# Kernel optimization log

Measured on AMD Instinct MI355X. Metric: run time of the kernel, lower is better.

Reference implementation:

```python
import jax, jax.numpy as jnp
import numpy as np

B, LP, LQ, D = 32, 2048, 512, 256

def setup_inputs() -> dict:
    key = jax.random.key(0)
    k1, k2, k3, k4 = jax.random.split(key, 4)
    x = jax.random.normal(k1, (B, LP, D), dtype=jnp.float32)
    y = jax.random.normal(k2, (B, LQ, D), dtype=jnp.float32)
    # nn.Linear(input_size, input_size): weight [D, D], bias [D]
    bound = 1.0 / np.sqrt(D)
    W = jax.random.uniform(k3, (D, D), minval=-bound, maxval=bound, dtype=jnp.float32)
    b = jax.random.uniform(k4, (D,), minval=-bound, maxval=bound, dtype=jnp.float32)
    return {"x": x, "y": y, "W": W, "b": b}

def reference(x, y, W, b):
    # shared linear + relu projection (torch Linear: x @ W.T + b)
    x_proj = jax.nn.relu(jnp.einsum('bpd,ed->bpe', x, W) + b)  # [B, LP, D]
    y_proj = jax.nn.relu(jnp.einsum('bqd,ed->bqe', y, W) + b)  # [B, LQ, D]
    # unscaled cross-attention scores
    scores = jnp.einsum('bpd,bqd->bpq', x_proj, y_proj)        # [B, LP, LQ]
    alpha = jax.nn.softmax(scores, axis=-1)
    # weighted sum over original (unprojected) y
    match_seq = jnp.einsum('bpq,bqd->bpd', alpha, y)           # [B, LP, D]
    return match_seq
```

## Files before the change

kernel.cpp:

```cpp
#include <hip/hip_runtime.h>
#include <stdint.h>

#define B_  32
#define LP_ 2048
#define LQ_ 512
#define D_  256

typedef __attribute__((ext_vector_type(8))) short short8;
typedef __attribute__((ext_vector_type(8))) _Float16 f16x8;
typedef __attribute__((ext_vector_type(4))) float f32x4;

__device__ __forceinline__ ushort f2h(float x) {
    union { _Float16 h; ushort u; } v;
    v.h = (_Float16)x;
    return v.u;
}
__device__ __forceinline__ void gl_lds16(const void* g, void* l) {
    __builtin_amdgcn_global_load_lds(
        (const __attribute__((address_space(1))) void*)g,
        (__attribute__((address_space(3))) void*)l, 16, 0, 0);
}


__global__ void k_prep(const float* __restrict__ W, const float* __restrict__ y,
                       ushort* __restrict__ Whf, ushort* __restrict__ yf) {
    __shared__ float t[32 * 260];
    if (blockIdx.x < 256) {
        int i = blockIdx.x * 256 + threadIdx.x;
        int e = i >> 8, k = i & 255;
        size_t off = (size_t)((k >> 5) * 16 + (e >> 4)) * 512 +
                     ((k >> 3) & 3) * 128 + (e & 15) * 8 + (k & 7);
        Whf[off] = f2h(W[i]);
        return;
    }
    int bid = blockIdx.x - 256;
    int b = bid >> 4, qc = bid & 15;
    int tid = threadIdx.x;
    int ql = tid >> 3;
    int d0 = (tid & 7) * 4;
#pragma unroll
    for (int p = 0; p < 8; p++) {
        int d = p * 32 + d0;
        float4 v = *(const float4*)(y + ((size_t)(b * LQ_ + qc * 32 + ql) * 256 + d));
        t[ql * 260 + d + 0] = v.x; t[ql * 260 + d + 1] = v.y;
        t[ql * 260 + d + 2] = v.z; t[ql * 260 + d + 3] = v.w;
    }
    __syncthreads();
    int w = tid >> 6, L = tid & 63, c = L & 15, quad = L >> 4;
#pragma unroll
    for (int ii = 0; ii < 4; ii++) {
        int nt = w * 4 + ii;
        short8 o;
#pragma unroll
        for (int j = 0; j < 8; j++)
            o[j] = (short)f2h(t[(quad * 8 + j) * 260 + nt * 16 + c]);
        *(short8*)(yf + ((size_t)(b * 256 + qc * 16 + nt) * 512 + L * 8)) = o;
    }
}

__global__ __launch_bounds__(256, 3) void k_proj(const float* __restrict__ x,
                                                 const float* __restrict__ y,
                                                 const ushort* __restrict__ Whf,
                                                 const float* __restrict__ bias,
                                                 ushort* __restrict__ Ox,
                                                 ushort* __restrict__ Oy) {
    __shared__ __align__(16) ushort Ws[16704];
    const int tid  = threadIdx.x;
    const int w    = tid >> 6;
    const int L    = tid & 63;
    const int c    = L & 15;
    const int quad = L >> 4;
    const bool isY = blockIdx.x < 256;
    const float* A = isY ? y : x;
    ushort* O      = isY ? Oy : Ox;
    const int blk0 = isY ? blockIdx.x : (blockIdx.x - 256);
    const int row0 = blk0 * 64 + w * 16;
    const int arow = row0 + c;

    f32x4 acc[16];
#pragma unroll
    for (int i = 0; i < 16; i++) acc[i] = (f32x4)0.f;

#define PSTAGE(kc, p)                                                          \
    {                                                                          \
        _Pragma("unroll")                                                      \
        for (int ii = 0; ii < 4; ii++) {                                       \
            int i = w * 4 + ii;                                                \
            gl_lds16(Whf + (size_t)(kc) * 8192 + i * 512 + L * 8,              \
                     (char*)Ws + (p) * 16384 + i * 1024);                      \
        }                                                                      \
    }

    PSTAGE(0, 0);
    float4 nx0 = *(const float4*)(A + (size_t)arow * 256 + quad * 8);
    float4 nx1 = *(const float4*)(A + (size_t)arow * 256 + quad * 8 + 4);

    for (int kc = 0; kc < 8; kc++) {
        __syncthreads();
        if (kc < 7) PSTAGE(kc + 1, (kc + 1) & 1);
        float4 cx0 = nx0, cx1 = nx1;
        if (kc < 7) {
            nx0 = *(const float4*)(A + (size_t)arow * 256 + (kc + 1) * 32 + quad * 8);
            nx1 = *(const float4*)(A + (size_t)arow * 256 + (kc + 1) * 32 + quad * 8 + 4);
        }
        float xs[8] = {cx0.x, cx0.y, cx0.z, cx0.w, cx1.x, cx1.y, cx1.z, cx1.w};
        f16x8 ah;
#pragma unroll
        for (int j = 0; j < 8; j++) ah[j] = (_Float16)xs[j];
        const ushort* buf = Ws + (kc & 1) * 8192;
#pragma unroll
        for (int nt = 0; nt < 16; nt++) {
            f16x8 bh = *(const f16x8*)(buf + nt * 512 + L * 8);
            acc[nt] = __builtin_amdgcn_mfma_f32_16x16x32_f16(ah, bh, acc[nt], 0, 0, 0);
        }
    }

    __syncthreads();
    float* tr = (float*)Ws + w * (16 * 130);
    const int rt_g = row0 >> 4;
#pragma unroll
    for (int half = 0; half < 2; half++) {
#pragma unroll
        for (int nt8 = 0; nt8 < 8; nt8++) {
            int nt = half * 8 + nt8;
            float bv = bias[nt * 16 + c];
#pragma unroll
            for (int r = 0; r < 4; r++)
                tr[(quad * 4 + r) * 130 + nt8 * 16 + c] = fmaxf(acc[nt][r] + bv, 0.f);
        }
#pragma unroll
        for (int ec4 = 0; ec4 < 4; ec4++) {
            int ec = half * 4 + ec4;
            short8 hh;
#pragma unroll
            for (int j = 0; j < 8; j++)
                hh[j] = (short)f2h(tr[c * 130 + ec4 * 32 + quad * 8 + j]);
            size_t blk = isY ? ((size_t)(rt_g >> 5) * 256 + ec * 32 + (rt_g & 31))
                             : ((size_t)rt_g * 8 + ec);
            *(short8*)(O + blk * 512 + L * 8) = hh;
        }
    }
}

__global__ __launch_bounds__(256, 4) void k_attn(const ushort* __restrict__ xpf,
                                                 const ushort* __restrict__ ypf,
                                                 const ushort* __restrict__ yf,
                                                 float* __restrict__ out) {
    __shared__ __align__(16) ushort lds[16384];
    const int tid  = threadIdx.x;
    const int w    = tid >> 6;
    const int L    = tid & 63;
    const int c    = L & 15;
    const int quad = L >> 4;

    const int bid = blockIdx.x;
    const int jj  = bid >> 3;
    const int b   = (bid & 7) * 4 + (jj >> 6);
    const int mt  = jj & 63;
    const int m0  = mt * 32;

#pragma unroll
    for (int ii = 0; ii < 4; ii++) {
        int unit = w * 4 + ii;
        int rs = unit >> 3, kc = unit & 7;
        gl_lds16(xpf + ((size_t)(b * 128 + mt * 2 + rs) * 8 + kc) * 512 + L * 8,
                 (char*)lds + unit * 1024);
    }

    f32x4 sc[2][8];
#pragma unroll
    for (int rs = 0; rs < 2; rs++)
#pragma unroll
        for (int qt = 0; qt < 8; qt++) sc[rs][qt] = (f32x4)0.f;
    __syncthreads();

    const ushort* yb = ypf + (size_t)b * 256 * 512;
    for (int kc = 0; kc < 8; kc++) {
        f16x8 ah0 = *(const f16x8*)(lds + kc * 512 + L * 8);
        f16x8 ah1 = *(const f16x8*)(lds + (8 + kc) * 512 + L * 8);
#pragma unroll
        for (int qt = 0; qt < 8; qt++) {
            f16x8 bh = *(const f16x8*)(yb + ((size_t)kc * 32 + w * 8 + qt) * 512 + L * 8);
            sc[0][qt] = __builtin_amdgcn_mfma_f32_16x16x32_f16(ah0, bh, sc[0][qt], 0, 0, 0);
            sc[1][qt] = __builtin_amdgcn_mfma_f32_16x16x32_f16(ah1, bh, sc[1][qt], 0, 0, 0);
        }
    }

    __syncthreads();
    float* red  = (float*)lds;
    float* red2 = red + 128;
    float inv[2][4];
#pragma unroll
    for (int rs = 0; rs < 2; rs++)
#pragma unroll
        for (int r = 0; r < 4; r++) {
            float pm = sc[rs][0][r];
#pragma unroll
            for (int qt = 1; qt < 8; qt++) pm = fmaxf(pm, sc[rs][qt][r]);
#pragma unroll
            for (int mask = 1; mask <= 8; mask <<= 1) pm = fmaxf(pm, __shfl_xor(pm, mask));
            if (c == 0) red[(rs * 16 + quad * 4 + r) * 4 + w] = pm;
        }
    __syncthreads();
#pragma unroll
    for (int rs = 0; rs < 2; rs++)
#pragma unroll
        for (int r = 0; r < 4; r++) {
            int row = rs * 16 + quad * 4 + r;
            float m = fmaxf(fmaxf(red[row * 4], red[row * 4 + 1]),
                            fmaxf(red[row * 4 + 2], red[row * 4 + 3]));
            float ps = 0.f;
#pragma unroll
            for (int qt = 0; qt < 8; qt++) {
                float e = __expf(sc[rs][qt][r] - m);
                sc[rs][qt][r] = e;
                ps += e;
            }
#pragma unroll
            for (int mask = 1; mask <= 8; mask <<= 1) ps += __shfl_xor(ps, mask);
            if (c == 0) red2[row * 4 + w] = ps;
        }
    __syncthreads();
#pragma unroll
    for (int rs = 0; rs < 2; rs++)
#pragma unroll
        for (int r = 0; r < 4; r++) {
            int row = rs * 16 + quad * 4 + r;
            inv[rs][r] = 1.f / (red2[row * 4] + red2[row * 4 + 1] +
                                red2[row * 4 + 2] + red2[row * 4 + 3]);
        }
    __syncthreads();

#pragma unroll
    for (int rs = 0; rs < 2; rs++)
#pragma unroll
        for (int r = 0; r < 4; r++) {
            int m_loc = rs * 16 + quad * 4 + r;
            int swz = m_loc & 7;
            float iv = inv[rs][r];
#pragma unroll
            for (int qt = 0; qt < 8; qt++) {
                int q = w * 128 + qt * 16 + c;
                lds[m_loc * 512 + (((q >> 3) ^ swz) << 3) + (c & 7)] = f2h(sc[rs][qt][r] * iv);
            }
        }
    __syncthreads();

    f32x4 o[2][4];
#pragma unroll
    for (int rs = 0; rs < 2; rs++)
#pragma unroll
        for (int dt = 0; dt < 4; dt++) o[rs][dt] = (f32x4)0.f;
    const int dh = w;
    const int swzA = c & 7;
    for (int kcq = 0; kcq < 16; kcq++) {
        int chunk = kcq * 4 + quad;
        f16x8 af0 = *(const f16x8*)(lds + c * 512 + ((chunk ^ swzA) << 3));
        f16x8 af1 = *(const f16x8*)(lds + (16 + c) * 512 + ((chunk ^ swzA) << 3));
        const ushort* ybf = yf + ((size_t)(b * 256 + kcq * 16 + dh * 4)) * 512;
#pragma unroll
        for (int dt = 0; dt < 4; dt++) {
            f16x8 bfr = *(const f16x8*)(ybf + dt * 512 + L * 8);
            o[0][dt] = __builtin_amdgcn_mfma_f32_16x16x32_f16(af0, bfr, o[0][dt], 0, 0, 0);
            o[1][dt] = __builtin_amdgcn_mfma_f32_16x16x32_f16(af1, bfr, o[1][dt], 0, 0, 0);
        }
    }

#pragma unroll
    for (int rs = 0; rs < 2; rs++)
#pragma unroll
        for (int dt = 0; dt < 4; dt++)
#pragma unroll
            for (int r = 0; r < 4; r++) {
                int row = rs * 16 + quad * 4 + r;
                out[(size_t)(b * LP_ + m0 + row) * 256 + dh * 64 + dt * 16 + c] =
                    o[rs][dt][r];
            }
}

extern "C" void kernel_launch(void* const* d_in, const int* in_sizes, int n_in,
                              void* d_out, int out_size, void* d_ws, size_t ws_size,
                              hipStream_t stream) {
    const float* x    = (const float*)d_in[0];
    const float* y    = (const float*)d_in[1];
    const float* W    = (const float*)d_in[2];
    const float* bias = (const float*)d_in[3];
    float* out = (float*)d_out;

    char* ws = (char*)d_ws;
    size_t off = 0;
    ushort* Whf = (ushort*)(ws + off); off += (size_t)D_ * D_ * 2;
    ushort* yfb = (ushort*)(ws + off); off += (size_t)B_ * D_ * LQ_ * 2;
    ushort* ypf = (ushort*)(ws + off); off += (size_t)B_ * LQ_ * D_ * 2;
    ushort* xpf = (ushort*)(ws + off); off += (size_t)B_ * LP_ * D_ * 2;

    k_prep<<<768, 256, 0, stream>>>(W, y, Whf, yfb);
    k_proj<<<1280, 256, 0, stream>>>(x, y, Whf, bias, xpf, ypf);
    k_attn<<<B_ * 64, 256, 0, stream>>>(xpf, ypf, yfb, out);
}
```

Measured before the change: 204.4 us.

## Fuse x projection into attention kernel, dropping xpf round trip

The x-side linear+ReLU projection now runs inside the attention kernel. Each block loads its 32 rows of x as fp32, converts them to fp16 in LDS, multiplies by the fp16 weight read from global memory with MFMA, applies bias and ReLU, and writes the projected tile to LDS for the score GEMM. This removes writing and re-reading the fp16 xpf buffer and shrinks k_proj to the y rows only. In exchange the attention kernel does more work per block, and every block streams the whole weight matrix from global/L2, which may raise register pressure and lengthen the prologue.

```diff
diff --git a/kernel.cpp b/kernel.cpp
--- a/kernel.cpp
+++ b/kernel.cpp
@@ -58,11 +58,9 @@
     }
 }
 
-__global__ __launch_bounds__(256, 3) void k_proj(const float* __restrict__ x,
-                                                 const float* __restrict__ y,
+__global__ __launch_bounds__(256, 3) void k_proj(const float* __restrict__ y,
                                                  const ushort* __restrict__ Whf,
                                                  const float* __restrict__ bias,
-                                                 ushort* __restrict__ Ox,
                                                  ushort* __restrict__ Oy) {
     __shared__ __align__(16) ushort Ws[16704];
     const int tid  = threadIdx.x;
@@ -70,11 +68,7 @@
     const int L    = tid & 63;
     const int c    = L & 15;
     const int quad = L >> 4;
-    const bool isY = blockIdx.x < 256;
-    const float* A = isY ? y : x;
-    ushort* O      = isY ? Oy : Ox;
-    const int blk0 = isY ? blockIdx.x : (blockIdx.x - 256);
-    const int row0 = blk0 * 64 + w * 16;
+    const int row0 = blockIdx.x * 64 + w * 16;
     const int arow = row0 + c;
 
     f32x4 acc[16];
@@ -92,16 +86,16 @@
     }
 
     PSTAGE(0, 0);
-    float4 nx0 = *(const float4*)(A + (size_t)arow * 256 + quad * 8);
-    float4 nx1 = *(const float4*)(A + (size_t)arow * 256 + quad * 8 + 4);
+    float4 nx0 = *(const float4*)(y + (size_t)arow * 256 + quad * 8);
+    float4 nx1 = *(const float4*)(y + (size_t)arow * 256 + quad * 8 + 4);
 
     for (int kc = 0; kc < 8; kc++) {
         __syncthreads();
         if (kc < 7) PSTAGE(kc + 1, (kc + 1) & 1);
         float4 cx0 = nx0, cx1 = nx1;
         if (kc < 7) {
-            nx0 = *(const float4*)(A + (size_t)arow * 256 + (kc + 1) * 32 + quad * 8);
-            nx1 = *(const float4*)(A + (size_t)arow * 256 + (kc + 1) * 32 + quad * 8 + 4);
+            nx0 = *(const float4*)(y + (size_t)arow * 256 + (kc + 1) * 32 + quad * 8);
+            nx1 = *(const float4*)(y + (size_t)arow * 256 + (kc + 1) * 32 + quad * 8 + 4);
         }
         float xs[8] = {cx0.x, cx0.y, cx0.z, cx0.w, cx1.x, cx1.y, cx1.z, cx1.w};
         f16x8 ah;
@@ -135,14 +129,15 @@
 #pragma unroll
             for (int j = 0; j < 8; j++)
                 hh[j] = (short)f2h(tr[c * 130 + ec4 * 32 + quad * 8 + j]);
-            size_t blk = isY ? ((size_t)(rt_g >> 5) * 256 + ec * 32 + (rt_g & 31))
-                             : ((size_t)rt_g * 8 + ec);
-            *(short8*)(O + blk * 512 + L * 8) = hh;
-        }
-    }
-}
-
-__global__ __launch_bounds__(256, 4) void k_attn(const ushort* __restrict__ xpf,
+            size_t blk = (size_t)(rt_g >> 5) * 256 + ec * 32 + (rt_g & 31);
+            *(short8*)(Oy + blk * 512 + L * 8) = hh;
+        }
+    }
+}
+
+__global__ __launch_bounds__(256, 4) void k_attn(const float* __restrict__ x,
+                                                 const ushort* __restrict__ Whf,
+                                                 const float* __restrict__ bias,
                                                  const ushort* __restrict__ ypf,
                                                  const ushort* __restrict__ yf,
                                                  float* __restrict__ out) {
@@ -163,8 +158,44 @@
     for (int ii = 0; ii < 4; ii++) {
         int unit = w * 4 + ii;
         int rs = unit >> 3, kc = unit & 7;
-        gl_lds16(xpf + ((size_t)(b * 128 + mt * 2 + rs) * 8 + kc) * 512 + L * 8,
-                 (char*)lds + unit * 1024);
+        const float* xs = x + ((size_t)(b * LP_ + m0 + rs * 16 + c)) * 256 + kc * 32 + quad * 8;
+        float4 v0 = *(const float4*)xs;
+        float4 v1 = *(const float4*)(xs + 4);
+        f16x8 h;
+        h[0] = (_Float16)v0.x; h[1] = (_Float16)v0.y;
+        h[2] = (_Float16)v0.z; h[3] = (_Float16)v0.w;
+        h[4] = (_Float16)v1.x; h[5] = (_Float16)v1.y;
+        h[6] = (_Float16)v1.z; h[7] = (_Float16)v1.w;
+        *(f16x8*)(lds + unit * 512 + L * 8) = h;
+    }
+    __syncthreads();
+
+    {
+        const int prs = w & 1, peh = w >> 1;
+        float bv[8];
+#pragma unroll
+        for (int ne = 0; ne < 8; ne++) bv[ne] = bias[(peh * 8 + ne) * 16 + c];
+        f32x4 pacc[8];
+#pragma unroll
+        for (int ne = 0; ne < 8; ne++) pacc[ne] = (f32x4)0.f;
+        for (int kc = 0; kc < 8; kc++) {
+            f16x8 ah = *(const f16x8*)(lds + (prs * 8 + kc) * 512 + L * 8);
+#pragma unroll
+            for (int ne = 0; ne < 8; ne++) {
+                f16x8 wb = *(const f16x8*)(Whf + ((size_t)(kc * 16 + peh * 8 + ne)) * 512 + L * 8);
+                pacc[ne] = __builtin_amdgcn_mfma_f32_16x16x32_f16(ah, wb, pacc[ne], 0, 0, 0);
+            }
+        }
+#pragma unroll
+        for (int ne = 0; ne < 8; ne++) {
+#pragma unroll
+            for (int r = 0; r < 4; r++) {
+                float v = fmaxf(pacc[ne][r] + bv[ne], 0.f);
+                int off = 8192 + (prs * 8 + peh * 4 + (ne >> 1)) * 512 +
+                          ((ne & 1) * 2 + (c >> 3)) * 128 + (quad * 4 + r) * 8 + (c & 7);
+                lds[off] = f2h(v);
+            }
+        }
     }
 
     f32x4 sc[2][8];
@@ -174,10 +205,11 @@
         for (int qt = 0; qt < 8; qt++) sc[rs][qt] = (f32x4)0.f;
     __syncthreads();
 
+    const ushort* pf = lds + 8192;
     const ushort* yb = ypf + (size_t)b * 256 * 512;
     for (int kc = 0; kc < 8; kc++) {
-        f16x8 ah0 = *(const f16x8*)(lds + kc * 512 + L * 8);
-        f16x8 ah1 = *(const f16x8*)(lds + (8 + kc) * 512 + L * 8);
+        f16x8 ah0 = *(const f16x8*)(pf + kc * 512 + L * 8);
+        f16x8 ah1 = *(const f16x8*)(pf + (8 + kc) * 512 + L * 8);
 #pragma unroll
         for (int qt = 0; qt < 8; qt++) {
             f16x8 bh = *(const f16x8*)(yb + ((size_t)kc * 32 + w * 8 + qt) * 512 + L * 8);
@@ -292,9 +324,8 @@
     ushort* Whf = (ushort*)(ws + off); off += (size_t)D_ * D_ * 2;
     ushort* yfb = (ushort*)(ws + off); off += (size_t)B_ * D_ * LQ_ * 2;
     ushort* ypf = (ushort*)(ws + off); off += (size_t)B_ * LQ_ * D_ * 2;
-    ushort* xpf = (ushort*)(ws + off); off += (size_t)B_ * LP_ * D_ * 2;
 
     k_prep<<<768, 256, 0, stream>>>(W, y, Whf, yfb);
-    k_proj<<<1280, 256, 0, stream>>>(x, y, Whf, bias, xpf, ypf);
-    k_attn<<<B_ * 64, 256, 0, stream>>>(xpf, ypf, yfb, out);
-}
+    k_proj<<<256, 256, 0, stream>>>(y, Whf, bias, ypf);
+    k_attn<<<B_ * 64, 256, 0, stream>>>(x, Whf, bias, ypf, yfb, out);
+}
```

Measured after the change: 203.0 us. Within noise of the previous version (-0.7%).
